# Optimization experiments

Hardware: AMD Instinct MI355X
Metric: run time of the kernel (lower is better)

The kernel has to match this reference:

```python
import jax, jax.numpy as jnp
import numpy as np


def _ln(x, g, b, eps=1e-5):
    mu = jnp.mean(x, axis=-1, keepdims=True)
    var = jnp.mean((x - mu) ** 2, axis=-1, keepdims=True)
    return (x - mu) * jax.lax.rsqrt(var + eps) * g + b


def setup_inputs() -> dict:
    key = jax.random.key(0)
    ks = jax.random.split(key, 12)
    B, H, W, D = 16, 128, 128, 64
    N = H * W
    Dff = 4 * D
    s = 0.02
    f32 = jnp.float32
    return {
        "x": jax.random.normal(ks[0], (B, N, D), f32),
        "H": H,
        "W": W,
        "ln1_scale": jnp.ones((D,), f32),
        "ln1_bias": jnp.zeros((D,), f32),
        "Wk": jax.random.normal(ks[1], (D, D), f32) * s,
        "bk": jnp.zeros((D,), f32),
        "Wq": jax.random.normal(ks[2], (D, D), f32) * s,
        "bq": jnp.zeros((D,), f32),
        "Wv": jax.random.normal(ks[3], (D, D), f32) * s,
        "bv": jnp.zeros((D,), f32),
        "Wr": jax.random.normal(ks[4], (D, D), f32) * s,
        "br": jnp.zeros((D,), f32),
        "ln2_scale": jnp.ones((D,), f32),
        "ln2_bias": jnp.zeros((D,), f32),
        "W1": jax.random.normal(ks[5], (Dff, D), f32) * s,
        "b1": jnp.zeros((Dff,), f32),
        "dw_w": jax.random.normal(ks[6], (Dff, 1, 3, 3), f32) * s,
        "dw_b": jnp.zeros((Dff,), f32),
        "W2": jax.random.normal(ks[7], (D, Dff), f32) * s,
        "b2": jnp.zeros((D,), f32),
    }


def reference(x, H, W, ln1_scale, ln1_bias, Wk, bk, Wq, bq, Wv, bv, Wr, br,
              ln2_scale, ln2_bias, W1, b1, dw_w, dw_b, W2, b2):
    B, N, D = x.shape
    Dff = W1.shape[0]

    # ---- EfficientAttention (head_count=1), tokens kept as [B, N, C] ----
    n1 = _ln(x, ln1_scale, ln1_bias)
    # 1x1 convs on [B,D,H,W] == per-token linear projections
    k = jax.nn.softmax(n1 @ Wk.T + bk, axis=1)    # softmax over spatial dim N (torch dim=2 of [B,Ck,N])
    q = jax.nn.softmax(n1 @ Wq.T + bq, axis=-1)   # softmax over key channels (torch dim=1)
    v = n1 @ Wv.T + bv                            # [B,N,Cv]
    context = jnp.einsum('bnk,bnv->bkv', k, v)    # key @ value^T, tiny [B,Ck,Cv]
    att = jnp.einsum('bkv,bnk->bnv', context, q)  # context^T @ query -> [B,N,Cv]
    attn_out = att @ Wr.T + br                    # reprojection 1x1 conv
    tx = x + attn_out

    # ---- MixFFN: fc1 -> depthwise 3x3 -> GELU -> fc2 ----
    n2 = _ln(tx, ln2_scale, ln2_bias)
    h = n2 @ W1.T + b1                            # [B,N,Dff]
    himg = jnp.transpose(h, (0, 2, 1)).reshape(B, Dff, H, W)
    conv = jax.lax.conv_general_dilated(
        himg, dw_w, window_strides=(1, 1), padding='SAME',
        feature_group_count=Dff,
        dimension_numbers=('NCHW', 'OIHW', 'NCHW')) + dw_b[None, :, None, None]
    h2 = jnp.transpose(conv.reshape(B, Dff, N), (0, 2, 1))
    h2 = jax.nn.gelu(h2, approximate=False)       # torch nn.GELU default is exact erf
    out = tx + (h2 @ W2.T + b2)
    return out
```

## Files before the change

### kernel.cpp

```cpp
#include <hip/hip_runtime.h>
#include <math.h>

typedef __bf16 bf16x8 __attribute__((ext_vector_type(8)));
typedef float f32x4 __attribute__((ext_vector_type(4)));
typedef unsigned short u16x8 __attribute__((ext_vector_type(8)));
typedef unsigned short u16x4v __attribute__((ext_vector_type(4)));

constexpr int NIMG = 16384;
constexpr int HPITCH = 130;
constexpr int HROW = HPITCH*256;

__device__ __forceinline__ unsigned short f2bf(float f){
  unsigned u = __builtin_bit_cast(unsigned, f);
  u += 0x7fffu + ((u>>16)&1u);
  return (unsigned short)(u>>16);
}
__device__ __forceinline__ unsigned pack2(float a, float b){
  return (unsigned)f2bf(a) | ((unsigned)f2bf(b)<<16);
}
__device__ __forceinline__ float bf2f(unsigned short h){
  unsigned u = ((unsigned)h)<<16;
  return __builtin_bit_cast(float, u);
}
__device__ __forceinline__ bf16x8 ldfrag_g(const unsigned short* p){
  u16x8 v = *reinterpret_cast<const u16x8*>(p);
  return __builtin_bit_cast(bf16x8, v);
}
__device__ __forceinline__ f32x4 mfma16(bf16x8 a, bf16x8 b, f32x4 c){
  return __builtin_amdgcn_mfma_f32_16x16x32_bf16(a, b, c, 0, 0, 0);
}
__device__ __forceinline__ f32x4 bfcvt4(uint2 q){
  f32x4 r;
  r[0] = __builtin_bit_cast(float, q.x << 16);
  r[1] = __builtin_bit_cast(float, q.x & 0xffff0000u);
  r[2] = __builtin_bit_cast(float, q.y << 16);
  r[3] = __builtin_bit_cast(float, q.y & 0xffff0000u);
  return r;
}

__global__ __launch_bounds__(64) void k0_wfrag(
  const float* __restrict__ Wk, const float* __restrict__ Wq,
  const float* __restrict__ Wv, const float* __restrict__ Wr,
  const float* __restrict__ W1, const float* __restrict__ W2,
  const float* __restrict__ dww, float* __restrict__ dwp,
  unsigned short* __restrict__ wf)
{
  const int bid = blockIdx.x, l = threadIdx.x;
  if (bid == 96){
    #pragma unroll
    for (int c=0;c<4;++c){
      int f = l*4 + c;
      #pragma unroll
      for (int j=0;j<9;++j) dwp[l*36 + j*4 + c] = dww[f*9+j];
    }
    return;
  }
  const float* src; int K, nt, ks; unsigned short* dst;
  if (bid < 32){
    int w = bid>>3, f = bid&7;
    src = (w==0)?Wk:(w==1)?Wq:(w==2)?Wv:Wr;
    K = 64; nt = f>>1; ks = f&1;
    dst = wf + w*4096 + f*512;
  } else if (bid < 64){
    int f = bid-32; src = W1; K = 64; nt = f>>1; ks = f&1;
    dst = wf + 16384 + f*512;
  } else {
    int f = bid-64; src = W2; K = 256; nt = f>>3; ks = f&7;
    dst = wf + 32768 + f*512;
  }
  u16x8 v;
  #pragma unroll
  for (int j=0;j<8;++j){
    int k = ks*32 + (l>>4)*8 + j;
    int n = nt*16 + (l&15);
    v[j] = f2bf(src[n*K + k]);
  }
  *reinterpret_cast<u16x8*>(dst + l*8) = v;
}

__global__ __launch_bounds__(256) void zhalo(unsigned* __restrict__ gh, unsigned* __restrict__ zr){
  int idx = blockIdx.x*256 + threadIdx.x;
  if (idx < 524288){
    int ch2 = idx & 127;
    int pos = idx >> 7;
    int side = pos & 1, row = pos >> 1;
    gh[(size_t)(row*HPITCH + side*(HPITCH-1))*128 + ch2] = 0;
  } else {
    int j = idx - 524288;
    if (j < HROW/2) zr[j] = 0;
  }
}

__global__ __launch_bounds__(256,2) void k1_ctx(
  const float* __restrict__ x, const float* __restrict__ g1, const float* __restrict__ be1,
  const float* __restrict__ bk, const float* __restrict__ bv,
  const unsigned short* __restrict__ wf,
  float* __restrict__ g_part, float* __restrict__ g_sump)
{
  __shared__ unsigned short tiles[4][4096];
  __shared__ float ctx_l[64*68];
  __shared__ float ssum_l[4][64];
  const int t = threadIdx.x, wid = t>>6, l = t&63;
  const int lg = l>>4, l15 = l&15;
  unsigned short* tile = tiles[wid];
  const int tok0 = blockIdx.x*512 + wid*128;

  bf16x8 WkF[8], WvF[8];
  #pragma unroll
  for (int f=0; f<8; ++f){
    WkF[f] = ldfrag_g(wf +    0 + f*512 + l*8);
    WvF[f] = ldfrag_g(wf + 8192 + f*512 + l*8);
  }
  float4 g1v  = *reinterpret_cast<const float4*>(&g1[l15*4]);
  float4 be1v = *reinterpret_cast<const float4*>(&be1[l15*4]);
  float bkv[4], bvv[4];
  #pragma unroll
  for (int ct=0; ct<4; ++ct){ bkv[ct]=bk[ct*16+l15]; bvv[ct]=bv[ct*16+l15]; }

  f32x4 acc[4][4];
  #pragma unroll
  for (int a=0;a<4;++a)
    #pragma unroll
    for (int b=0;b<4;++b) acc[a][b] = (f32x4){0.f,0.f,0.f,0.f};
  float sume[4] = {0.f,0.f,0.f,0.f};

  for (int tb=0; tb<2; ++tb){
    const int tbase = tok0 + tb*64;
    #pragma unroll
    for (int it=0; it<16; ++it){
      int row = it*4 + lg;
      float4 xv = *reinterpret_cast<const float4*>(&x[(size_t)(tbase+row)*64 + l15*4]);
      float s1 = xv.x+xv.y+xv.z+xv.w;
      float s2 = xv.x*xv.x + xv.y*xv.y + xv.z*xv.z + xv.w*xv.w;
      #pragma unroll
      for (int off=1; off<16; off<<=1){ s1 += __shfl_xor(s1,off,64); s2 += __shfl_xor(s2,off,64); }
      float mu = s1*(1.f/64.f);
      float rs = rsqrtf(s2*(1.f/64.f) - mu*mu + 1e-5f);
      uint2 pk = { pack2((xv.x-mu)*rs*g1v.x + be1v.x, (xv.y-mu)*rs*g1v.y + be1v.y),
                   pack2((xv.z-mu)*rs*g1v.z + be1v.z, (xv.w-mu)*rs*g1v.w + be1v.w) };
      *reinterpret_cast<uint2*>(&tile[row*64 + ((l15*4) ^ ((row&7)<<3))]) = pk;
    }
    bf16x8 aF[4][2];
    #pragma unroll
    for (int mt=0;mt<4;++mt){
      int row = mt*16+l15, sw=(row&7)<<3, ab=row*64;
      aF[mt][0] = __builtin_bit_cast(bf16x8, *reinterpret_cast<const u16x8*>(tile+ab+((     lg*8)^sw)));
      aF[mt][1] = __builtin_bit_cast(bf16x8, *reinterpret_cast<const u16x8*>(tile+ab+((32 + lg*8)^sw)));
    }
    #pragma unroll
    for (int half=0; half<2; ++half){
      #pragma unroll
      for (int m2=0;m2<2;++m2){
        const int mt = half*2+m2;
        #pragma unroll
        for (int ct=0;ct<4;++ct){
          f32x4 z = {0.f,0.f,0.f,0.f};
          z = mfma16(aF[mt][0], WkF[ct*2+0], z);
          z = mfma16(aF[mt][1], WkF[ct*2+1], z);
          float e0=__expf(z[0]+bkv[ct]), e1=__expf(z[1]+bkv[ct]);
          float e2=__expf(z[2]+bkv[ct]), e3=__expf(z[3]+bkv[ct]);
          sume[ct] += (e0+e1)+(e2+e3);
          const int c = ct*16+l15, sw = (c&7)<<3;
          const int cb = m2*16+lg*4;
          uint2 pe = { pack2(e0,e1), pack2(e2,e3) };
          *reinterpret_cast<uint2*>(&tile[c*64 + (cb ^ sw)]) = pe;
          f32x4 w = {0.f,0.f,0.f,0.f};
          w = mfma16(aF[mt][0], WvF[ct*2+0], w);
          w = mfma16(aF[mt][1], WvF[ct*2+1], w);
          uint2 pv = { pack2(w[0]+bvv[ct], w[1]+bvv[ct]), pack2(w[2]+bvv[ct], w[3]+bvv[ct]) };
          *reinterpret_cast<uint2*>(&tile[c*64 + ((32+cb) ^ sw)]) = pv;
        }
      }
      bf16x8 eA[4], vB[4];
      #pragma unroll
      for (int cm=0;cm<4;++cm){
        int row = cm*16+l15, sw=(row&7)<<3;
        eA[cm] = __builtin_bit_cast(bf16x8, *reinterpret_cast<const u16x8*>(tile + row*64 + ((     lg*8)^sw)));
        vB[cm] = __builtin_bit_cast(bf16x8, *reinterpret_cast<const u16x8*>(tile + row*64 + ((32 + lg*8)^sw)));
      }
      #pragma unroll
      for (int cm=0; cm<4; ++cm)
        #pragma unroll
        for (int jn=0; jn<4; ++jn)
          acc[cm][jn] = mfma16(eA[cm], vB[jn], acc[cm][jn]);
    }
  }
  #pragma unroll
  for (int ct=0; ct<4; ++ct){
    float s = sume[ct];
    s += __shfl_xor(s,16,64); s += __shfl_xor(s,32,64);
    if (lg==0) ssum_l[wid][ct*16+l15] = s;
  }
  #define CTX_RED(OP) \
    _Pragma("unroll") for (int cm=0;cm<4;++cm) \
    _Pragma("unroll") for (int jn=0;jn<4;++jn) \
    _Pragma("unroll") for (int r=0;r<4;++r) \
      ctx_l[(cm*16+lg*4+r)*68 + jn*16+l15] OP acc[cm][jn][r];
  if (wid==0){ CTX_RED(=) }  __syncthreads();
  if (wid==1){ CTX_RED(+=) } __syncthreads();
  if (wid==2){ CTX_RED(+=) } __syncthreads();
  if (wid==3){ CTX_RED(+=) } __syncthreads();
  #undef CTX_RED
  for (int i=t; i<4096; i+=256)
    g_part[(size_t)blockIdx.x*4096 + i] = ctx_l[(i>>6)*68 + (i&63)];
  if (t<64)
    g_sump[blockIdx.x*64 + t] = ssum_l[0][t]+ssum_l[1][t]+ssum_l[2][t]+ssum_l[3][t];
}

__global__ __launch_bounds__(512) void k15_ctxwr(
  const float* __restrict__ g_part, const float* __restrict__ g_sump,
  const float* __restrict__ Wr, unsigned short* __restrict__ ctxWrF)
{
  __shared__ float sctx[4096];
  __shared__ float sWr[4096];
  __shared__ float sinv[64];
  const int b = blockIdx.x, t = threadIdx.x;
  if (t<64){
    float s=0.f;
    #pragma unroll 8
    for (int p=0;p<32;++p) s += g_sump[(b*32+p)*64 + t];
    sinv[t] = 1.f/s;
  }
  for (int idx=t; idx<4096; idx+=512){
    float s=0.f;
    #pragma unroll 8
    for (int p=0;p<32;++p) s += g_part[(size_t)(b*32+p)*4096 + idx];
    sctx[idx] = s;
  }
  __syncthreads();
  {
    int c = t>>3, d0 = (t&7)*8;
    float invc = sinv[c];
    #pragma unroll
    for (int dd=0; dd<8; ++dd){
      int d = d0+dd; float s = 0.f;
      #pragma unroll
      for (int v=0; v<64; ++v) s += sctx[c*64+v]*Wr[d*64+v];
      sWr[c*64+d] = s*invc;
    }
  }
  __syncthreads();
  {
    int f = t>>6, l = t&63, nt = f>>1, ks = f&1;
    u16x8 v;
    #pragma unroll
    for (int j=0;j<8;++j){
      int k = ks*32 + (l>>4)*8 + j;
      int n = nt*16 + (l&15);
      v[j] = f2bf(sWr[k*64+n]);
    }
    *reinterpret_cast<u16x8*>(ctxWrF + b*4096 + f*512 + l*8) = v;
  }
}

__global__ __launch_bounds__(256,2) void k2_attn_ffn1(
  const float* __restrict__ x,
  const float* __restrict__ g1, const float* __restrict__ be1,
  const float* __restrict__ bq, const float* __restrict__ br,
  const float* __restrict__ g2, const float* __restrict__ be2,
  const float* __restrict__ b1,
  const unsigned short* __restrict__ wf,
  const unsigned short* __restrict__ ctxWrF,
  unsigned short* __restrict__ g_txb, unsigned short* __restrict__ g_h)
{
  __shared__ unsigned short tiles[4][4096];
  const int t = threadIdx.x, wid = t>>6, l = t&63;
  const int l15 = l&15, lg = l>>4;
  unsigned short* tile = tiles[wid];
  const int tok0 = (blockIdx.x*4 + wid)*64;
  const int img  = blockIdx.x>>6;
  const int yrow = (tok0>>7)&127;
  const int xb   = tok0&127;
  const size_t hbase = ((size_t)(img*128 + yrow)*HPITCH + 1 + xb)*256;

  bf16x8 WqF[8], CWF[8];
  #pragma unroll
  for (int f=0; f<8; ++f){
    WqF[f] = ldfrag_g(wf + 4096 + f*512 + l*8);
    CWF[f] = ldfrag_g(ctxWrF + img*4096 + f*512 + l*8);
  }
  float4 g1v  = *reinterpret_cast<const float4*>(&g1[l15*4]);
  float4 be1v = *reinterpret_cast<const float4*>(&be1[l15*4]);
  float bqv[4], brv[4], g2v[4], be2v[4];
  #pragma unroll
  for (int nt=0; nt<4; ++nt){
    bqv[nt]=bq[nt*16+l15]; brv[nt]=br[nt*16+l15];
    g2v[nt]=g2[nt*16+l15]; be2v[nt]=be2[nt*16+l15];
  }
  float b1v[16];
  #pragma unroll
  for (int i=0;i<16;++i) b1v[i]=b1[i*16+l15];

  #pragma unroll
  for (int it=0; it<16; ++it){
    int row = it*4 + lg;
    float4 xv = *reinterpret_cast<const float4*>(&x[(size_t)(tok0+row)*64 + l15*4]);
    float s1 = xv.x+xv.y+xv.z+xv.w;
    float s2 = xv.x*xv.x + xv.y*xv.y + xv.z*xv.z + xv.w*xv.w;
    #pragma unroll
    for (int off=1; off<16; off<<=1){ s1 += __shfl_xor(s1,off,64); s2 += __shfl_xor(s2,off,64); }
    float mu = s1*(1.f/64.f);
    float rs = rsqrtf(s2*(1.f/64.f) - mu*mu + 1e-5f);
    uint2 pk = { pack2((xv.x-mu)*rs*g1v.x + be1v.x, (xv.y-mu)*rs*g1v.y + be1v.y),
                 pack2((xv.z-mu)*rs*g1v.z + be1v.z, (xv.w-mu)*rs*g1v.w + be1v.w) };
    *reinterpret_cast<uint2*>(&tile[row*64 + ((l15*4) ^ ((row&7)<<3))]) = pk;
  }

  for (int mt=0; mt<4; ++mt){
    const int arow = mt*16 + l15;
    const int asw  = (arow&7)<<3;
    const int abase= arow*64;
    bf16x8 a0 = __builtin_bit_cast(bf16x8, *reinterpret_cast<const u16x8*>(tile + abase + ((     lg*8) ^ asw)));
    bf16x8 a1 = __builtin_bit_cast(bf16x8, *reinterpret_cast<const u16x8*>(tile + abase + ((32 + lg*8) ^ asw)));
    f32x4 qa[4];
    #pragma unroll
    for (int nt=0; nt<4; ++nt){
      f32x4 z = {0.f,0.f,0.f,0.f};
      z = mfma16(a0, WqF[nt*2+0], z);
      z = mfma16(a1, WqF[nt*2+1], z);
      qa[nt] = z;
    }
    #pragma unroll
    for (int nt=0; nt<4; ++nt)
      #pragma unroll
      for (int r=0; r<4; ++r) qa[nt][r] += bqv[nt];
    float mx[4];
    #pragma unroll
    for (int r=0;r<4;++r) mx[r] = fmaxf(fmaxf(qa[0][r],qa[1][r]), fmaxf(qa[2][r],qa[3][r]));
    #pragma unroll
    for (int off=1; off<16; off<<=1)
      #pragma unroll
      for (int r=0;r<4;++r) mx[r] = fmaxf(mx[r], __shfl_xor(mx[r], off, 64));
    float sm[4] = {0.f,0.f,0.f,0.f};
    #pragma unroll
    for (int nt=0;nt<4;++nt)
      #pragma unroll
      for (int r=0;r<4;++r){ float e = __expf(qa[nt][r]-mx[r]); qa[nt][r]=e; sm[r]+=e; }
    #pragma unroll
    for (int off=1; off<16; off<<=1)
      #pragma unroll
      for (int r=0;r<4;++r) sm[r] += __shfl_xor(sm[r], off, 64);
    float inv[4];
    #pragma unroll
    for (int r=0;r<4;++r) inv[r] = 1.f/sm[r];
    #pragma unroll
    for (int nt=0;nt<4;++nt)
      #pragma unroll
      for (int r=0;r<4;++r){
        int row = mt*16 + lg*4 + r, col = nt*16 + l15;
        tile[row*64 + (col ^ ((row&7)<<3))] = f2bf(qa[nt][r]*inv[r]);
      }
    bf16x8 p0 = __builtin_bit_cast(bf16x8, *reinterpret_cast<const u16x8*>(tile + abase + ((     lg*8) ^ asw)));
    bf16x8 p1 = __builtin_bit_cast(bf16x8, *reinterpret_cast<const u16x8*>(tile + abase + ((32 + lg*8) ^ asw)));
    f32x4 ao[4];
    #pragma unroll
    for (int nt=0; nt<4; ++nt){
      f32x4 z = {0.f,0.f,0.f,0.f};
      z = mfma16(p0, CWF[nt*2+0], z);
      z = mfma16(p1, CWF[nt*2+1], z);
      ao[nt] = z;
    }
    float txv[4][4];
    float s1v[4] = {0.f,0.f,0.f,0.f}, s2v[4] = {0.f,0.f,0.f,0.f};
    #pragma unroll
    for (int nt=0;nt<4;++nt)
      #pragma unroll
      for (int r=0;r<4;++r){
        size_t row = (size_t)(tok0 + mt*16 + lg*4 + r);
        float v = ao[nt][r] + brv[nt] + x[row*64 + nt*16+l15];
        g_txb[row*64 + nt*16+l15] = f2bf(v);
        txv[nt][r] = v; s1v[r] += v; s2v[r] += v*v;
      }
    #pragma unroll
    for (int off=1; off<16; off<<=1)
      #pragma unroll
      for (int r=0;r<4;++r){ s1v[r] += __shfl_xor(s1v[r], off, 64); s2v[r] += __shfl_xor(s2v[r], off, 64); }
    #pragma unroll
    for (int r=0;r<4;++r){
      float mu2 = s1v[r]*(1.f/64.f);
      float rs  = rsqrtf(s2v[r]*(1.f/64.f) - mu2*mu2 + 1e-5f);
      s1v[r] = mu2; s2v[r] = rs;
    }
    #pragma unroll
    for (int nt=0;nt<4;++nt)
      #pragma unroll
      for (int r=0;r<4;++r){
        int row = mt*16 + lg*4 + r, col = nt*16 + l15;
        float n2 = (txv[nt][r]-s1v[r])*s2v[r]*g2v[nt] + be2v[nt];
        tile[row*64 + (col ^ ((row&7)<<3))] = f2bf(n2);
      }
  }

  #pragma unroll 2
  for (int nt2=0; nt2<16; ++nt2){
    bf16x8 w0 = ldfrag_g(wf + 16384 + (nt2*2+0)*512 + l*8);
    bf16x8 w1 = ldfrag_g(wf + 16384 + (nt2*2+1)*512 + l*8);
    float bb = b1v[nt2];
    #pragma unroll
    for (int mt=0; mt<4; ++mt){
      const int arow = mt*16 + l15;
      const int asw  = (arow&7)<<3;
      const int abase= arow*64;
      bf16x8 n20 = __builtin_bit_cast(bf16x8, *reinterpret_cast<const u16x8*>(tile + abase + ((     lg*8) ^ asw)));
      bf16x8 n21 = __builtin_bit_cast(bf16x8, *reinterpret_cast<const u16x8*>(tile + abase + ((32 + lg*8) ^ asw)));
      f32x4 h = {bb,bb,bb,bb};
      h = mfma16(n20, w0, h);
      h = mfma16(n21, w1, h);
      #pragma unroll
      for (int r=0;r<4;++r)
        g_h[hbase + (size_t)(mt*16+lg*4+r)*256 + nt2*16 + l15] = f2bf(h[r]);
    }
  }
}

__global__ __launch_bounds__(256,4) void k3_conv_ffn2(
  const unsigned short* __restrict__ g_h,
  const unsigned short* __restrict__ zrow,
  const float* __restrict__ dwp, const float* __restrict__ dwb,
  const float* __restrict__ b2,
  const unsigned short* __restrict__ wf,
  const unsigned short* __restrict__ g_txb, float* __restrict__ out)
{
  __shared__ unsigned short tiles[4][4096];
  const int t = threadIdx.x, wid = t>>6, l = t&63;
  const int l15 = l&15, lg = l>>4;
  unsigned short* tile = tiles[wid];
  const int strip = (blockIdx.x & 7)*512 + (blockIdx.x >> 3);
  const int tok0 = strip*64;
  const int img  = tok0>>14;
  const int y    = (tok0>>7)&127;
  const int x0   = tok0&127;
  const bool okm = (y>0), okp = (y<127);
  const int p    = lg;
  const int ch   = l15;

  const f32x4 kC0 = {-2.3022082f,-2.3022082f,-2.3022082f,-2.3022082f};
  const f32x4 kC1 = {-0.1029432f,-0.1029432f,-0.1029432f,-0.1029432f};
  const f32x4 kOne = {1.f,1.f,1.f,1.f};

  const int f0 = wid*64 + ch*4;
  f32x4 cw4[9];
  #pragma unroll
  for (int j=0;j<9;++j)
    cw4[j] = *reinterpret_cast<const f32x4*>(&dwp[(wid*16+ch)*36 + j*4]);
  float4 cb4 = *reinterpret_cast<const float4*>(&dwb[f0]);
  f32x4 cbv = {cb4.x, cb4.y, cb4.z, cb4.w};

  const size_t base = ((size_t)(img*128+y)*HPITCH + x0 + p*16)*256;
  const unsigned short* rB = g_h + base + f0;
  const unsigned short* rA = okm ? (rB - HROW) : (zrow + f0);
  const unsigned short* rC = okp ? (rB + HROW) : (zrow + f0);

  auto ldr = [](const unsigned short* pp, int o) -> uint2 {
    return *reinterpret_cast<const uint2*>(pp + o*256);
  };

  f32x4 PA=bfcvt4(ldr(rA,0)), PB=bfcvt4(ldr(rB,0)), PC=bfcvt4(ldr(rC,0));
  f32x4 CA=bfcvt4(ldr(rA,1)), CB=bfcvt4(ldr(rB,1)), CC=bfcvt4(ldr(rC,1));
  uint2 r2A=ldr(rA,2), r2B=ldr(rB,2), r2C=ldr(rC,2);
  uint2 r3A=ldr(rA,3), r3B=ldr(rB,3), r3C=ldr(rC,3);
  uint2 r4A=ldr(rA,4), r4B=ldr(rB,4), r4C=ldr(rC,4);

  #pragma unroll 4
  for (int s=0; s<16; ++s){
    const int o = (s<13) ? (s+5) : 17;
    uint2 r5A=ldr(rA,o), r5B=ldr(rB,o), r5C=ldr(rC,o);
    f32x4 NA=bfcvt4(r2A), NB=bfcvt4(r2B), NC=bfcvt4(r2C);
    f32x4 a = cbv;
    a += cw4[0]*PA; a += cw4[1]*CA; a += cw4[2]*NA;
    a += cw4[3]*PB; a += cw4[4]*CB; a += cw4[5]*NB;
    a += cw4[6]*PC; a += cw4[7]*CC; a += cw4[8]*NC;
    f32x4 u = a*a;
    f32x4 w = u*kC1 + kC0;
    f32x4 arg = a*w;
    f32x4 e;
    e[0]=__builtin_amdgcn_exp2f(arg[0]); e[1]=__builtin_amdgcn_exp2f(arg[1]);
    e[2]=__builtin_amdgcn_exp2f(arg[2]); e[3]=__builtin_amdgcn_exp2f(arg[3]);
    f32x4 den = e + kOne;
    f32x4 rc;
    rc[0]=__builtin_amdgcn_rcpf(den[0]); rc[1]=__builtin_amdgcn_rcpf(den[1]);
    rc[2]=__builtin_amdgcn_rcpf(den[2]); rc[3]=__builtin_amdgcn_rcpf(den[3]);
    f32x4 g = a*rc;
    unsigned lo, hi;
    asm("v_cvt_pk_bf16_f32 %0, %1, %2" : "=v"(lo) : "v"(g[0]), "v"(g[1]));
    asm("v_cvt_pk_bf16_f32 %0, %1, %2" : "=v"(hi) : "v"(g[2]), "v"(g[3]));
    uint2 pk = { lo, hi };
    int row = p*16 + s;
    *reinterpret_cast<uint2*>(&tile[row*64 + ((ch*4) ^ ((row&7)<<3))]) = pk;
    PA=CA; PB=CB; PC=CC; CA=NA; CB=NB; CC=NC;
    r2A=r3A; r2B=r3B; r2C=r3C;
    r3A=r4A; r3B=r4B; r3C=r4C;
    r4A=r5A; r4B=r5B; r4C=r5C;
  }

  u16x4v tq[4];
  #pragma unroll
  for (int mtk=0;mtk<4;++mtk)
    tq[mtk] = *reinterpret_cast<const u16x4v*>(
        &g_txb[(size_t)(tok0 + mtk*16 + l15)*64 + wid*16 + lg*4]);
  bf16x8 W2F[8];
  #pragma unroll
  for (int q=0;q<8;++q){
    int i2 = q>>1, cks = q&1;
    W2F[q] = ldfrag_g(wf + 32768 + (wid*8 + i2*2 + cks)*512 + l*8);
  }

  __syncthreads();

  f32x4 oacc[4];
  #pragma unroll
  for (int mtk=0;mtk<4;++mtk) oacc[mtk] = (f32x4){0.f,0.f,0.f,0.f};
  #pragma unroll
  for (int i=0;i<4;++i){
    const unsigned short* tp = tiles[i];
    #pragma unroll
    for (int mtk=0; mtk<4; ++mtk){
      int row = mtk*16 + l15;
      int sw = (row&7)<<3;
      bf16x8 fb0 = __builtin_bit_cast(bf16x8, *reinterpret_cast<const u16x8*>(tp + row*64 + ((     lg*8) ^ sw)));
      bf16x8 fb1 = __builtin_bit_cast(bf16x8, *reinterpret_cast<const u16x8*>(tp + row*64 + ((32 + lg*8) ^ sw)));
      oacc[mtk] = mfma16(W2F[i*2+0], fb0, oacc[mtk]);
      oacc[mtk] = mfma16(W2F[i*2+1], fb1, oacc[mtk]);
    }
  }

  float4 b2q = *reinterpret_cast<const float4*>(&b2[wid*16 + lg*4]);
  #pragma unroll
  for (int mtk=0;mtk<4;++mtk){
    const size_t off = (size_t)(tok0 + mtk*16 + l15)*64 + wid*16 + lg*4;
    float4 o;
    o.x = oacc[mtk][0] + b2q.x + bf2f(tq[mtk][0]);
    o.y = oacc[mtk][1] + b2q.y + bf2f(tq[mtk][1]);
    o.z = oacc[mtk][2] + b2q.z + bf2f(tq[mtk][2]);
    o.w = oacc[mtk][3] + b2q.w + bf2f(tq[mtk][3]);
    *reinterpret_cast<float4*>(&out[off]) = o;
  }
}

extern "C" void kernel_launch(void* const* d_in, const int* in_sizes, int n_in,
                              void* d_out, int out_size, void* d_ws, size_t ws_size,
                              hipStream_t stream)
{
  const float* x  =(const float*)d_in[0];
  const float* g1 =(const float*)d_in[3];
  const float* be1=(const float*)d_in[4];
  const float* Wk =(const float*)d_in[5];
  const float* bk =(const float*)d_in[6];
  const float* Wq =(const float*)d_in[7];
  const float* bq =(const float*)d_in[8];
  const float* Wv =(const float*)d_in[9];
  const float* bv =(const float*)d_in[10];
  const float* Wr =(const float*)d_in[11];
  const float* br =(const float*)d_in[12];
  const float* g2 =(const float*)d_in[13];
  const float* be2=(const float*)d_in[14];
  const float* W1 =(const float*)d_in[15];
  const float* b1 =(const float*)d_in[16];
  const float* dww=(const float*)d_in[17];
  const float* dwb=(const float*)d_in[18];
  const float* W2 =(const float*)d_in[19];
  const float* b2 =(const float*)d_in[20];
  float* outp = (float*)d_out;
  char* ws = (char*)d_ws;

  unsigned short* wfb    = (unsigned short*)ws;
  unsigned short* ctxWrF = (unsigned short*)(ws + 98304);
  float* g_sump = (float*)(ws + 229376);
  float* g_part = (float*)(ws + 393216);
  unsigned short* g_txb = (unsigned short*)(ws + 16777216);
  unsigned short* g_h   = (unsigned short*)(ws + 50331648);
  unsigned short* zr    = (unsigned short*)(ws + 186646528);
  float* dwp            = (float*)(ws + 186712064);

  hipLaunchKernelGGL(k0_wfrag, dim3(97), dim3(64), 0, stream, Wk, Wq, Wv, Wr, W1, W2, dww, dwp, wfb);
  hipLaunchKernelGGL(zhalo, dim3(2113), dim3(256), 0, stream, (unsigned*)g_h, (unsigned*)zr);
  hipLaunchKernelGGL(k1_ctx, dim3(512), dim3(256), 0, stream, x, g1, be1, bk, bv, wfb, g_part, g_sump);
  hipLaunchKernelGGL(k15_ctxwr, dim3(16), dim3(512), 0, stream, g_part, g_sump, Wr, ctxWrF);
  hipLaunchKernelGGL(k2_attn_ffn1, dim3(1024), dim3(256), 0, stream,
                     x, g1, be1, bq, br, g2, be2, b1, wfb, ctxWrF, g_txb, g_h);
  hipLaunchKernelGGL(k3_conv_ffn2, dim3(4096), dim3(256), 0, stream,
                     g_h, zr, dwp, dwb, b2, wfb, g_txb, outp);
}
```

Measured before the change: 251.4 us.

## Permute FFN hidden channel layout to vectorize h stores and shrink conv blocks

The FFN1 epilogue now packs pairs of output tiles so each lane writes 16 contiguous bf16 channels with two 128-bit stores, using a permuted channel order for g_h. The depthwise conv + FFN2 kernel is restructured: 128-thread blocks each handle 16 tokens across all 256 channels (2 channels per thread), with W2 rows and conv weights/bias pre-permuted in k0 to match the new layout. This targets scattered 2-byte global stores and improves occupancy. In exchange it launches four times as many blocks, has W2 fragments loaded per block, and puts more pressure on the shared tile.

```diff
diff --git a/kernel.cpp b/kernel.cpp
--- a/kernel.cpp
+++ b/kernel.cpp
@@ -3,6 +3,7 @@
 
 typedef __bf16 bf16x8 __attribute__((ext_vector_type(8)));
 typedef float f32x4 __attribute__((ext_vector_type(4)));
+typedef float f32x2 __attribute__((ext_vector_type(2)));
 typedef unsigned short u16x8 __attribute__((ext_vector_type(8)));
 typedef unsigned short u16x4v __attribute__((ext_vector_type(4)));
 
@@ -29,33 +30,38 @@
 __device__ __forceinline__ f32x4 mfma16(bf16x8 a, bf16x8 b, f32x4 c){
   return __builtin_amdgcn_mfma_f32_16x16x32_bf16(a, b, c, 0, 0, 0);
 }
-__device__ __forceinline__ f32x4 bfcvt4(uint2 q){
-  f32x4 r;
-  r[0] = __builtin_bit_cast(float, q.x << 16);
-  r[1] = __builtin_bit_cast(float, q.x & 0xffff0000u);
-  r[2] = __builtin_bit_cast(float, q.y << 16);
-  r[3] = __builtin_bit_cast(float, q.y & 0xffff0000u);
+__device__ __forceinline__ f32x2 bfcvt2(unsigned q){
+  f32x2 r;
+  r[0] = __builtin_bit_cast(float, q << 16);
+  r[1] = __builtin_bit_cast(float, q & 0xffff0000u);
   return r;
 }
+
 
 __global__ __launch_bounds__(64) void k0_wfrag(
   const float* __restrict__ Wk, const float* __restrict__ Wq,
   const float* __restrict__ Wv, const float* __restrict__ Wr,
   const float* __restrict__ W1, const float* __restrict__ W2,
-  const float* __restrict__ dww, float* __restrict__ dwp,
-  unsigned short* __restrict__ wf)
+  const float* __restrict__ dww, const float* __restrict__ dwb,
+  float* __restrict__ dwp, unsigned short* __restrict__ wf)
 {
   const int bid = blockIdx.x, l = threadIdx.x;
   if (bid == 96){
     #pragma unroll
-    for (int c=0;c<4;++c){
-      int f = l*4 + c;
-      #pragma unroll
-      for (int j=0;j<9;++j) dwp[l*36 + j*4 + c] = dww[f*9+j];
+    for (int h=0; h<2; ++h){
+      int tt = l + h*64;
+      #pragma unroll
+      for (int jc=0; jc<2; ++jc){
+        int cp = tt*2 + jc;
+        int f = ((cp&15)<<4) | (cp>>4);
+        #pragma unroll
+        for (int j=0;j<9;++j) dwp[tt*20 + j*2 + jc] = dww[f*9+j];
+        dwp[tt*20 + 18 + jc] = dwb[f];
+      }
     }
     return;
   }
-  const float* src; int K, nt, ks; unsigned short* dst;
+  const float* src; int K, nt, ks; unsigned short* dst; bool perm = false;
   if (bid < 32){
     int w = bid>>3, f = bid&7;
     src = (w==0)?Wk:(w==1)?Wq:(w==2)?Wv:Wr;
@@ -66,12 +72,13 @@
     dst = wf + 16384 + f*512;
   } else {
     int f = bid-64; src = W2; K = 256; nt = f>>3; ks = f&7;
-    dst = wf + 32768 + f*512;
+    dst = wf + 32768 + f*512; perm = true;
   }
   u16x8 v;
   #pragma unroll
   for (int j=0;j<8;++j){
     int k = ks*32 + (l>>4)*8 + j;
+    if (perm) k = ((k&15)<<4) | (k>>4);
     int n = nt*16 + (l&15);
     v[j] = f2bf(src[n*K + k]);
   }
@@ -391,148 +398,144 @@
       }
   }
 
-  #pragma unroll 2
-  for (int nt2=0; nt2<16; ++nt2){
-    bf16x8 w0 = ldfrag_g(wf + 16384 + (nt2*2+0)*512 + l*8);
-    bf16x8 w1 = ldfrag_g(wf + 16384 + (nt2*2+1)*512 + l*8);
-    float bb = b1v[nt2];
-    #pragma unroll
-    for (int mt=0; mt<4; ++mt){
-      const int arow = mt*16 + l15;
-      const int asw  = (arow&7)<<3;
-      const int abase= arow*64;
-      bf16x8 n20 = __builtin_bit_cast(bf16x8, *reinterpret_cast<const u16x8*>(tile + abase + ((     lg*8) ^ asw)));
-      bf16x8 n21 = __builtin_bit_cast(bf16x8, *reinterpret_cast<const u16x8*>(tile + abase + ((32 + lg*8) ^ asw)));
-      f32x4 h = {bb,bb,bb,bb};
-      h = mfma16(n20, w0, h);
-      h = mfma16(n21, w1, h);
-      #pragma unroll
-      for (int r=0;r<4;++r)
-        g_h[hbase + (size_t)(mt*16+lg*4+r)*256 + nt2*16 + l15] = f2bf(h[r]);
-    }
-  }
-}
-
-__global__ __launch_bounds__(256,4) void k3_conv_ffn2(
+  for (int mt=0; mt<4; ++mt){
+    const int arow = mt*16 + l15;
+    const int asw  = (arow&7)<<3;
+    const int abase= arow*64;
+    bf16x8 n20 = __builtin_bit_cast(bf16x8, *reinterpret_cast<const u16x8*>(tile + abase + ((     lg*8) ^ asw)));
+    bf16x8 n21 = __builtin_bit_cast(bf16x8, *reinterpret_cast<const u16x8*>(tile + abase + ((32 + lg*8) ^ asw)));
+    unsigned hpk[4][8];
+    #pragma unroll
+    for (int np=0; np<8; ++np){
+      bf16x8 wa0 = ldfrag_g(wf + 16384 + (np*4+0)*512 + l*8);
+      bf16x8 wa1 = ldfrag_g(wf + 16384 + (np*4+1)*512 + l*8);
+      bf16x8 wb0 = ldfrag_g(wf + 16384 + (np*4+2)*512 + l*8);
+      bf16x8 wb1 = ldfrag_g(wf + 16384 + (np*4+3)*512 + l*8);
+      float ba = b1v[np*2], bb = b1v[np*2+1];
+      f32x4 ha = {ba,ba,ba,ba};
+      ha = mfma16(n20, wa0, ha);
+      ha = mfma16(n21, wa1, ha);
+      f32x4 hb = {bb,bb,bb,bb};
+      hb = mfma16(n20, wb0, hb);
+      hb = mfma16(n21, wb1, hb);
+      #pragma unroll
+      for (int r=0;r<4;++r) hpk[r][np] = pack2(ha[r], hb[r]);
+    }
+    #pragma unroll
+    for (int r=0;r<4;++r){
+      const size_t ro = hbase + (size_t)(mt*16+lg*4+r)*256 + l15*16;
+      uint4 v0 = { hpk[r][0], hpk[r][1], hpk[r][2], hpk[r][3] };
+      uint4 v1 = { hpk[r][4], hpk[r][5], hpk[r][6], hpk[r][7] };
+      *reinterpret_cast<uint4*>(&g_h[ro])   = v0;
+      *reinterpret_cast<uint4*>(&g_h[ro+8]) = v1;
+    }
+  }
+}
+
+__global__ __launch_bounds__(128,6) void k3_conv_ffn2(
   const unsigned short* __restrict__ g_h,
   const unsigned short* __restrict__ zrow,
-  const float* __restrict__ dwp, const float* __restrict__ dwb,
+  const float* __restrict__ dwp,
   const float* __restrict__ b2,
   const unsigned short* __restrict__ wf,
   const unsigned short* __restrict__ g_txb, float* __restrict__ out)
 {
-  __shared__ unsigned short tiles[4][4096];
-  const int t = threadIdx.x, wid = t>>6, l = t&63;
+  __shared__ unsigned short tile[4096];
+  const int t = threadIdx.x, wv = t>>6, l = t&63;
   const int l15 = l&15, lg = l>>4;
-  unsigned short* tile = tiles[wid];
-  const int strip = (blockIdx.x & 7)*512 + (blockIdx.x >> 3);
-  const int tok0 = strip*64;
+  const int blk = (blockIdx.x & 7)*2048 + (blockIdx.x >> 3);
+  const int tok0 = blk*16;
   const int img  = tok0>>14;
   const int y    = (tok0>>7)&127;
   const int x0   = tok0&127;
   const bool okm = (y>0), okp = (y<127);
-  const int p    = lg;
-  const int ch   = l15;
-
-  const f32x4 kC0 = {-2.3022082f,-2.3022082f,-2.3022082f,-2.3022082f};
-  const f32x4 kC1 = {-0.1029432f,-0.1029432f,-0.1029432f,-0.1029432f};
-  const f32x4 kOne = {1.f,1.f,1.f,1.f};
-
-  const int f0 = wid*64 + ch*4;
-  f32x4 cw4[9];
+
+  f32x2 cw[9];
   #pragma unroll
   for (int j=0;j<9;++j)
-    cw4[j] = *reinterpret_cast<const f32x4*>(&dwp[(wid*16+ch)*36 + j*4]);
-  float4 cb4 = *reinterpret_cast<const float4*>(&dwb[f0]);
-  f32x4 cbv = {cb4.x, cb4.y, cb4.z, cb4.w};
-
-  const size_t base = ((size_t)(img*128+y)*HPITCH + x0 + p*16)*256;
-  const unsigned short* rB = g_h + base + f0;
-  const unsigned short* rA = okm ? (rB - HROW) : (zrow + f0);
-  const unsigned short* rC = okp ? (rB + HROW) : (zrow + f0);
-
-  auto ldr = [](const unsigned short* pp, int o) -> uint2 {
-    return *reinterpret_cast<const uint2*>(pp + o*256);
+    cw[j] = *reinterpret_cast<const f32x2*>(&dwp[t*20 + j*2]);
+  f32x2 cb2 = *reinterpret_cast<const f32x2*>(&dwp[t*20 + 18]);
+
+  const size_t base = ((size_t)(img*128+y)*HPITCH + x0)*256;
+  const unsigned short* rB = g_h + base + t*2;
+  const unsigned short* rA = okm ? (rB - HROW) : (zrow + t*2);
+  const unsigned short* rC = okp ? (rB + HROW) : (zrow + t*2);
+
+  auto ldr = [](const unsigned short* pp, int o) -> unsigned {
+    return *reinterpret_cast<const unsigned*>(pp + o*256);
   };
 
-  f32x4 PA=bfcvt4(ldr(rA,0)), PB=bfcvt4(ldr(rB,0)), PC=bfcvt4(ldr(rC,0));
-  f32x4 CA=bfcvt4(ldr(rA,1)), CB=bfcvt4(ldr(rB,1)), CC=bfcvt4(ldr(rC,1));
-  uint2 r2A=ldr(rA,2), r2B=ldr(rB,2), r2C=ldr(rC,2);
-  uint2 r3A=ldr(rA,3), r3B=ldr(rB,3), r3C=ldr(rC,3);
-  uint2 r4A=ldr(rA,4), r4B=ldr(rB,4), r4C=ldr(rC,4);
+  const f32x2 kC0 = {-2.3022082f,-2.3022082f};
+  const f32x2 kC1 = {-0.1029432f,-0.1029432f};
+
+  f32x2 PA=bfcvt2(ldr(rA,0)), PB=bfcvt2(ldr(rB,0)), PC=bfcvt2(ldr(rC,0));
+  f32x2 CA=bfcvt2(ldr(rA,1)), CB=bfcvt2(ldr(rB,1)), CC=bfcvt2(ldr(rC,1));
+  unsigned r2A=ldr(rA,2), r2B=ldr(rB,2), r2C=ldr(rC,2);
+  unsigned r3A=ldr(rA,3), r3B=ldr(rB,3), r3C=ldr(rC,3);
+  unsigned r4A=ldr(rA,4), r4B=ldr(rB,4), r4C=ldr(rC,4);
 
   #pragma unroll 4
   for (int s=0; s<16; ++s){
     const int o = (s<13) ? (s+5) : 17;
-    uint2 r5A=ldr(rA,o), r5B=ldr(rB,o), r5C=ldr(rC,o);
-    f32x4 NA=bfcvt4(r2A), NB=bfcvt4(r2B), NC=bfcvt4(r2C);
-    f32x4 a = cbv;
-    a += cw4[0]*PA; a += cw4[1]*CA; a += cw4[2]*NA;
-    a += cw4[3]*PB; a += cw4[4]*CB; a += cw4[5]*NB;
-    a += cw4[6]*PC; a += cw4[7]*CC; a += cw4[8]*NC;
-    f32x4 u = a*a;
-    f32x4 w = u*kC1 + kC0;
-    f32x4 arg = a*w;
-    f32x4 e;
+    unsigned r5A=ldr(rA,o), r5B=ldr(rB,o), r5C=ldr(rC,o);
+    f32x2 NA=bfcvt2(r2A), NB=bfcvt2(r2B), NC=bfcvt2(r2C);
+    f32x2 a = cb2;
+    a += cw[0]*PA; a += cw[1]*CA; a += cw[2]*NA;
+    a += cw[3]*PB; a += cw[4]*CB; a += cw[5]*NB;
+    a += cw[6]*PC; a += cw[7]*CC; a += cw[8]*NC;
+    f32x2 u = a*a;
+    f32x2 w = u*kC1 + kC0;
+    f32x2 arg = a*w;
+    f32x2 e;
     e[0]=__builtin_amdgcn_exp2f(arg[0]); e[1]=__builtin_amdgcn_exp2f(arg[1]);
-    e[2]=__builtin_amdgcn_exp2f(arg[2]); e[3]=__builtin_amdgcn_exp2f(arg[3]);
-    f32x4 den = e + kOne;
-    f32x4 rc;
+    f32x2 den = e + (f32x2){1.f,1.f};
+    f32x2 rc;
     rc[0]=__builtin_amdgcn_rcpf(den[0]); rc[1]=__builtin_amdgcn_rcpf(den[1]);
-    rc[2]=__builtin_amdgcn_rcpf(den[2]); rc[3]=__builtin_amdgcn_rcpf(den[3]);
-    f32x4 g = a*rc;
-    unsigned lo, hi;
-    asm("v_cvt_pk_bf16_f32 %0, %1, %2" : "=v"(lo) : "v"(g[0]), "v"(g[1]));
-    asm("v_cvt_pk_bf16_f32 %0, %1, %2" : "=v"(hi) : "v"(g[2]), "v"(g[3]));
-    uint2 pk = { lo, hi };
-    int row = p*16 + s;
-    *reinterpret_cast<uint2*>(&tile[row*64 + ((ch*4) ^ ((row&7)<<3))]) = pk;
+    f32x2 g = a*rc;
+    unsigned pk;
+    asm("v_cvt_pk_bf16_f32 %0, %1, %2" : "=v"(pk) : "v"(g[0]), "v"(g[1]));
+    *reinterpret_cast<unsigned*>(&tile[s*256 + ((t*2) ^ ((s&7)<<3))]) = pk;
     PA=CA; PB=CB; PC=CC; CA=NA; CB=NB; CC=NC;
     r2A=r3A; r2B=r3B; r2C=r3C;
     r3A=r4A; r3B=r4B; r3C=r4C;
     r4A=r5A; r4B=r5B; r4C=r5C;
   }
 
-  u16x4v tq[4];
-  #pragma unroll
-  for (int mtk=0;mtk<4;++mtk)
-    tq[mtk] = *reinterpret_cast<const u16x4v*>(
-        &g_txb[(size_t)(tok0 + mtk*16 + l15)*64 + wid*16 + lg*4]);
-  bf16x8 W2F[8];
-  #pragma unroll
-  for (int q=0;q<8;++q){
-    int i2 = q>>1, cks = q&1;
-    W2F[q] = ldfrag_g(wf + 32768 + (wid*8 + i2*2 + cks)*512 + l*8);
-  }
-
   __syncthreads();
 
-  f32x4 oacc[4];
-  #pragma unroll
-  for (int mtk=0;mtk<4;++mtk) oacc[mtk] = (f32x4){0.f,0.f,0.f,0.f};
+  f32x4 oacc0 = {0.f,0.f,0.f,0.f};
+  f32x4 oacc1 = {0.f,0.f,0.f,0.f};
+  const int ntcA = wv*2, ntcB = wv*2+1;
   #pragma unroll
   for (int i=0;i<4;++i){
-    const unsigned short* tp = tiles[i];
-    #pragma unroll
-    for (int mtk=0; mtk<4; ++mtk){
-      int row = mtk*16 + l15;
-      int sw = (row&7)<<3;
-      bf16x8 fb0 = __builtin_bit_cast(bf16x8, *reinterpret_cast<const u16x8*>(tp + row*64 + ((     lg*8) ^ sw)));
-      bf16x8 fb1 = __builtin_bit_cast(bf16x8, *reinterpret_cast<const u16x8*>(tp + row*64 + ((32 + lg*8) ^ sw)));
-      oacc[mtk] = mfma16(W2F[i*2+0], fb0, oacc[mtk]);
-      oacc[mtk] = mfma16(W2F[i*2+1], fb1, oacc[mtk]);
-    }
-  }
-
-  float4 b2q = *reinterpret_cast<const float4*>(&b2[wid*16 + lg*4]);
-  #pragma unroll
-  for (int mtk=0;mtk<4;++mtk){
-    const size_t off = (size_t)(tok0 + mtk*16 + l15)*64 + wid*16 + lg*4;
+    const int n = l15;
+    const int nsw = (n&7)<<3;
+    const int cb0 = (i*64      + lg*8) ^ nsw;
+    const int cb1 = (i*64 + 32 + lg*8) ^ nsw;
+    bf16x8 fb0 = __builtin_bit_cast(bf16x8, *reinterpret_cast<const u16x8*>(&tile[n*256 + cb0]));
+    bf16x8 fb1 = __builtin_bit_cast(bf16x8, *reinterpret_cast<const u16x8*>(&tile[n*256 + cb1]));
+    bf16x8 WA0 = ldfrag_g(wf + 32768 + (ntcA*8 + i*2+0)*512 + l*8);
+    bf16x8 WA1 = ldfrag_g(wf + 32768 + (ntcA*8 + i*2+1)*512 + l*8);
+    bf16x8 WB0 = ldfrag_g(wf + 32768 + (ntcB*8 + i*2+0)*512 + l*8);
+    bf16x8 WB1 = ldfrag_g(wf + 32768 + (ntcB*8 + i*2+1)*512 + l*8);
+    oacc0 = mfma16(WA0, fb0, oacc0);
+    oacc0 = mfma16(WA1, fb1, oacc0);
+    oacc1 = mfma16(WB0, fb0, oacc1);
+    oacc1 = mfma16(WB1, fb1, oacc1);
+  }
+
+  #pragma unroll
+  for (int q=0;q<2;++q){
+    const int ntc = wv*2+q;
+    const size_t off = (size_t)(tok0 + l15)*64 + ntc*16 + lg*4;
+    u16x4v tq = *reinterpret_cast<const u16x4v*>(&g_txb[off]);
+    float4 b2q = *reinterpret_cast<const float4*>(&b2[ntc*16 + lg*4]);
+    f32x4 oc = q ? oacc1 : oacc0;
     float4 o;
-    o.x = oacc[mtk][0] + b2q.x + bf2f(tq[mtk][0]);
-    o.y = oacc[mtk][1] + b2q.y + bf2f(tq[mtk][1]);
-    o.z = oacc[mtk][2] + b2q.z + bf2f(tq[mtk][2]);
-    o.w = oacc[mtk][3] + b2q.w + bf2f(tq[mtk][3]);
+    o.x = oc[0] + b2q.x + bf2f(tq[0]);
+    o.y = oc[1] + b2q.y + bf2f(tq[1]);
+    o.z = oc[2] + b2q.z + bf2f(tq[2]);
+    o.w = oc[3] + b2q.w + bf2f(tq[3]);
     *reinterpret_cast<float4*>(&out[off]) = o;
   }
 }
@@ -572,12 +575,12 @@
   unsigned short* zr    = (unsigned short*)(ws + 186646528);
   float* dwp            = (float*)(ws + 186712064);
 
-  hipLaunchKernelGGL(k0_wfrag, dim3(97), dim3(64), 0, stream, Wk, Wq, Wv, Wr, W1, W2, dww, dwp, wfb);
+  hipLaunchKernelGGL(k0_wfrag, dim3(97), dim3(64), 0, stream, Wk, Wq, Wv, Wr, W1, W2, dww, dwb, dwp, wfb);
   hipLaunchKernelGGL(zhalo, dim3(2113), dim3(256), 0, stream, (unsigned*)g_h, (unsigned*)zr);
   hipLaunchKernelGGL(k1_ctx, dim3(512), dim3(256), 0, stream, x, g1, be1, bk, bv, wfb, g_part, g_sump);
   hipLaunchKernelGGL(k15_ctxwr, dim3(16), dim3(512), 0, stream, g_part, g_sump, Wr, ctxWrF);
   hipLaunchKernelGGL(k2_attn_ffn1, dim3(1024), dim3(256), 0, stream,
                      x, g1, be1, bq, br, g2, be2, b1, wfb, ctxWrF, g_txb, g_h);
-  hipLaunchKernelGGL(k3_conv_ffn2, dim3(4096), dim3(256), 0, stream,
-                     g_h, zr, dwp, dwb, b2, wfb, g_txb, outp);
-}
+  hipLaunchKernelGGL(k3_conv_ffn2, dim3(16384), dim3(128), 0, stream,
+                     g_h, zr, dwp, b2, wfb, g_txb, outp);
+}
```

Result: no change. 248.0 us (-1.3%).
